# Optimization experiments

Measured on AMD Instinct MI355X. Metric: run time of the kernel, lower is better.

## Reference

```python
import jax, jax.numpy as jnp
import numpy as np

N_NODES = 50000
N_EDGES = 800000
NUM_HEADS = 4
HEAD_DIM = 32
IN_DIM = 128
NEG_SLOPE = 0.2


def setup_inputs() -> dict:
    key = jax.random.key(0)
    k1, k2, k3, k4, k5, k6 = jax.random.split(key, 6)
    x = jax.random.normal(k1, (N_NODES, IN_DIM), dtype=jnp.float32)
    W = jax.random.normal(k2, (NUM_HEADS * HEAD_DIM, IN_DIM), dtype=jnp.float32) * 0.05
    attn_l = jax.random.normal(k3, (NUM_HEADS, HEAD_DIM), dtype=jnp.float32) * 0.05
    attn_r = jax.random.normal(k4, (NUM_HEADS, HEAD_DIM), dtype=jnp.float32) * 0.05
    src = jax.random.randint(k5, (N_EDGES,), 0, N_NODES, dtype=jnp.int32)
    dst = jnp.sort(jax.random.randint(k6, (N_EDGES,), 0, N_NODES, dtype=jnp.int32))
    return {"x": x, "W": W, "attn_l": attn_l, "attn_r": attn_r, "src": src, "dst": dst}


def reference(x, W, attn_l, attn_r, src, dst):
    N = x.shape[0]
    H, D = attn_l.shape
    # linear projection: [N, H*D] -> [N, H, D]
    feat = (x @ W.T).reshape(N, H, D)
    # per-node attention terms  [N, H]
    el = jnp.einsum('nhd,hd->nh', feat, attn_l)
    er = jnp.einsum('nhd,hd->nh', feat, attn_r)
    # per-edge logits (u_add_v) + leaky relu  [E, H]
    e = el[src] + er[dst]
    e = jnp.where(e > 0, e, NEG_SLOPE * e)
    # edge softmax segmented by destination node
    e_max = jax.ops.segment_max(e, dst, num_segments=N)          # [N, H]
    e_exp = jnp.exp(e - e_max[dst])                              # [E, H]
    denom = jax.ops.segment_sum(e_exp, dst, num_segments=N)     # [N, H]
    alpha = e_exp / denom[dst]                                   # [E, H]
    # attention-weighted neighbor aggregation  [N, H, D]
    out = jax.ops.segment_sum(alpha[:, :, None] * feat[src], dst, num_segments=N)
    return out.reshape(N, H * D)
```

## Files before the change

kernel.cpp:

```cpp
#include <hip/hip_runtime.h>
#include <math.h>

#define NN 50000
#define NE 800000
#define NH 4
#define HD 32
#define FD 128
#define NTILE 3125
#define GEMM_BLOCKS 256
#define ROWS_BLOCKS ((NE + 511) / 512)
#define CAP 1024

typedef __attribute__((ext_vector_type(8))) short short8;
typedef __attribute__((ext_vector_type(4))) float floatx4;

__device__ __forceinline__ unsigned short f2bf(float f) {
    union { float f; unsigned u; } v; v.f = f;
    unsigned u = v.u;
    return (unsigned short)((u + 0x7FFFu + ((u >> 16) & 1u)) >> 16);
}
__device__ __forceinline__ float bf_lo(unsigned u) {
    union { unsigned u; float f; } v; v.u = u << 16; return v.f;
}
__device__ __forceinline__ float bf_hi(unsigned u) {
    union { unsigned u; float f; } v; v.u = u & 0xFFFF0000u; return v.f;
}

__global__ __launch_bounds__(512) void k_gemm_rows(const float* __restrict__ x,
                                                   const float* __restrict__ W,
                                                   const float* __restrict__ al,
                                                   const float* __restrict__ ar,
                                                   const int* __restrict__ dst,
                                                   unsigned short* __restrict__ feat_bf,
                                                   float* __restrict__ el,
                                                   float* __restrict__ er,
                                                   int* __restrict__ rows) {
    const int tid = threadIdx.x;

    if (blockIdx.x >= GEMM_BLOCKS) {
        int e = (blockIdx.x - GEMM_BLOCKS) * 512 + tid;
        if (e < NE) {
            int dj = dst[e];
            if (e == 0) {
                for (int n = 0; n <= dj; ++n) rows[n] = 0;
            } else {
                int prev = dst[e - 1];
                for (int n = prev + 1; n <= dj; ++n) rows[n] = e;
            }
            if (e == NE - 1) {
                for (int n = dj + 1; n <= NN; ++n) rows[n] = NE;
            }
        }
        return;
    }

    __shared__ unsigned short Wl[FD * 136];
    for (int p = tid; p < FD * 64; p += 512) {
        int c = p >> 6, k2 = (p & 63) * 2;
        float2 wv = *(const float2*)&W[c * FD + k2];
        *(unsigned*)&Wl[c * 136 + k2] =
            (unsigned)f2bf(wv.x) | ((unsigned)f2bf(wv.y) << 16);
    }
    __syncthreads();

    const int wv_id = tid >> 6, lane = tid & 63;
    const int col = lane & 15, quad = lane >> 4;

    float alr[8], arr[8];
    #pragma unroll
    for (int ct = 0; ct < 8; ++ct) {
        alr[ct] = al[col + 16 * ct];
        arr[ct] = ar[col + 16 * ct];
    }

    for (int tile = blockIdx.x * 8 + wv_id; tile < NTILE; tile += GEMM_BLOCKS * 8) {
        const int n0 = tile * 16;

        short8 afrag[4];
        const float* xrow = x + (size_t)(n0 + col) * FD;
        #pragma unroll
        for (int s = 0; s < 4; ++s) {
            float4 u0 = *(const float4*)&xrow[s * 32 + quad * 8];
            float4 u1 = *(const float4*)&xrow[s * 32 + quad * 8 + 4];
            short8 a;
            a[0] = (short)f2bf(u0.x); a[1] = (short)f2bf(u0.y);
            a[2] = (short)f2bf(u0.z); a[3] = (short)f2bf(u0.w);
            a[4] = (short)f2bf(u1.x); a[5] = (short)f2bf(u1.y);
            a[6] = (short)f2bf(u1.z); a[7] = (short)f2bf(u1.w);
            afrag[s] = a;
        }

        floatx4 acc[8];
        #pragma unroll
        for (int ct = 0; ct < 8; ++ct) acc[ct] = (floatx4){0.f, 0.f, 0.f, 0.f};

        #pragma unroll
        for (int ct = 0; ct < 8; ++ct) {
            #pragma unroll
            for (int s = 0; s < 4; ++s) {
                short8 b = *(const short8*)&Wl[(ct * 16 + col) * 136 + s * 32 + quad * 8];
                acc[ct] = __builtin_amdgcn_mfma_f32_16x16x32_bf16(afrag[s], b, acc[ct], 0, 0, 0);
            }
        }

        #pragma unroll
        for (int ct = 0; ct < 8; ++ct) {
            #pragma unroll
            for (int r = 0; r < 4; ++r) {
                feat_bf[(size_t)(n0 + quad * 4 + r) * FD + ct * 16 + col] = f2bf(acc[ct][r]);
            }
        }

        #pragma unroll
        for (int r = 0; r < 4; ++r) {
            float ev[8];
            #pragma unroll
            for (int hh = 0; hh < NH; ++hh) {
                ev[hh]     = acc[2 * hh][r] * alr[2 * hh] + acc[2 * hh + 1][r] * alr[2 * hh + 1];
                ev[4 + hh] = acc[2 * hh][r] * arr[2 * hh] + acc[2 * hh + 1][r] * arr[2 * hh + 1];
            }
            #pragma unroll
            for (int m = 1; m < 16; m <<= 1) {
                #pragma unroll
                for (int j = 0; j < 8; ++j) ev[j] += __shfl_xor(ev[j], m);
            }
            if (col == 0) {
                int n = n0 + quad * 4 + r;
                *(float4*)&el[n * NH] = make_float4(ev[0], ev[1], ev[2], ev[3]);
                *(float4*)&er[n * NH] = make_float4(ev[4], ev[5], ev[6], ev[7]);
            }
        }
    }
}

__global__ __launch_bounds__(256) void k_aggregate(const unsigned short* __restrict__ feat_bf,
                                                   const float* __restrict__ el,
                                                   const float* __restrict__ er,
                                                   const int* __restrict__ src,
                                                   const int* __restrict__ dst,
                                                   const int* __restrict__ rows,
                                                   float* __restrict__ out) {
    __shared__ float wS[CAP * NH];
    const int tid = threadIdx.x;
    const int wave = tid >> 6;
    const int lane = tid & 63;
    const int n0 = blockIdx.x * 4;
    const int n  = n0 + wave;

    const int s0 = __builtin_amdgcn_readfirstlane(rows[n0]);
    const int t3 = __builtin_amdgcn_readfirstlane(rows[n0 + 4]);
    const int s  = __builtin_amdgcn_readfirstlane(rows[n]);
    const int t  = __builtin_amdgcn_readfirstlane(rows[n + 1]);

    const int q  = lane >> 4;
    const int lp = lane & 15;
    const int h  = lp >> 2;
    const int dimoff = 8 * lp;

    float acc[8] = {0.f, 0.f, 0.f, 0.f, 0.f, 0.f, 0.f, 0.f};
    float den = 0.f;

    for (int c0 = s0; c0 < t3; c0 += CAP) {
        const int c1 = min(c0 + CAP, t3);

        for (int e = c0 + tid; e < c1; e += 256) {
            int sj = src[e], dj = dst[e];
            float4 l4 = *(const float4*)&el[sj * NH];
            float4 r4 = *(const float4*)&er[dj * NH];
            float4 w; float lg;
            lg = l4.x + r4.x; w.x = __expf(fmaxf(lg, 0.2f * lg));
            lg = l4.y + r4.y; w.y = __expf(fmaxf(lg, 0.2f * lg));
            lg = l4.z + r4.z; w.z = __expf(fmaxf(lg, 0.2f * lg));
            lg = l4.w + r4.w; w.w = __expf(fmaxf(lg, 0.2f * lg));
            *(float4*)&wS[(e - c0) * NH] = w;
        }
        __syncthreads();

        const int sb = max(s, c0), tb = min(t, c1);
        for (int e = (sb & ~3); e < tb; e += 16) {
            const int base = e + 4 * q;
            int sj4[4];
            const bool full4 = (base >= sb) && (base + 3 < tb);
            if (full4) {
                int4 sv = *(const int4*)&src[base];
                sj4[0] = sv.x; sj4[1] = sv.y; sj4[2] = sv.z; sj4[3] = sv.w;
            } else {
                #pragma unroll
                for (int u = 0; u < 4; ++u) {
                    int ei = base + u;
                    sj4[u] = (ei >= sb && ei < tb) ? src[ei] : 0;
                }
            }

            float wv4[4];
            uint4 uvv[4];
            #pragma unroll
            for (int u = 0; u < 4; ++u) {
                int ei = base + u;
                bool v = (ei >= sb) && (ei < tb);
                wv4[u] = v ? wS[(ei - c0) * NH + h] : 0.f;
                if (v) uvv[u] = *(const uint4*)&feat_bf[(size_t)sj4[u] * FD + dimoff];
            }

            #pragma unroll
            for (int u = 0; u < 4; ++u) {
                int ei = base + u;
                if (ei >= sb && ei < tb) {
                    float w = wv4[u];
                    uint4 uv = uvv[u];
                    acc[0] += w * bf_lo(uv.x); acc[1] += w * bf_hi(uv.x);
                    acc[2] += w * bf_lo(uv.y); acc[3] += w * bf_hi(uv.y);
                    acc[4] += w * bf_lo(uv.z); acc[5] += w * bf_hi(uv.z);
                    acc[6] += w * bf_lo(uv.w); acc[7] += w * bf_hi(uv.w);
                    den += w;
                }
            }
        }
        __syncthreads();
    }

    #pragma unroll
    for (int m = 16; m < 64; m <<= 1) {
        #pragma unroll
        for (int j = 0; j < 8; ++j) acc[j] += __shfl_xor(acc[j], m);
        den += __shfl_xor(den, m);
    }

    if (q == 0) {
        const float rden = (den > 0.f) ? 1.f / den : 0.f;
        float* op = out + (size_t)n * FD + dimoff;
        *(float4*)op       = make_float4(acc[0] * rden, acc[1] * rden, acc[2] * rden, acc[3] * rden);
        *(float4*)(op + 4) = make_float4(acc[4] * rden, acc[5] * rden, acc[6] * rden, acc[7] * rden);
    }
}

extern "C" void kernel_launch(void* const* d_in, const int* in_sizes, int n_in,
                              void* d_out, int out_size, void* d_ws, size_t ws_size,
                              hipStream_t stream) {
    const float* x  = (const float*)d_in[0];
    const float* W  = (const float*)d_in[1];
    const float* al = (const float*)d_in[2];
    const float* ar = (const float*)d_in[3];
    const int* src  = (const int*)d_in[4];
    const int* dst  = (const int*)d_in[5];
    float* out = (float*)d_out;

    unsigned short* feat_bf = (unsigned short*)d_ws;
    float* el = (float*)(feat_bf + (size_t)NN * FD);
    float* er = el + (size_t)NN * NH;
    int*   rows = (int*)(er + (size_t)NN * NH);

    k_gemm_rows<<<GEMM_BLOCKS + ROWS_BLOCKS, 512, 0, stream>>>(x, W, al, ar, dst,
                                                               feat_bf, el, er, rows);
    k_aggregate<<<NN / 4, 256, 0, stream>>>(feat_bf, el, er, src, dst, rows, out);
}
```

Baseline: 136.3 us.

## Fold attention vectors into projection MFMA, cache src indices in LDS

Precomputes W^T·attn_l and W^T·attn_r as an extra bf16 weight tile in shared memory, so el/er come from one extra MFMA per tile instead of a shuffle reduction. The GEMM block count is doubled to spread the tiles across more blocks. The aggregation kernel stores src indices in LDS during the weight pass, which removes the repeated global src reads and the alignment branches. The cost is an extra per-block precompute of the folded weights, more LDS, and slightly different rounding because the folded attention weights are held in bf16.

```diff
diff --git a/kernel.cpp b/kernel.cpp
--- a/kernel.cpp
+++ b/kernel.cpp
@@ -7,7 +7,7 @@
 #define HD 32
 #define FD 128
 #define NTILE 3125
-#define GEMM_BLOCKS 256
+#define GEMM_BLOCKS 512
 #define ROWS_BLOCKS ((NE + 511) / 512)
 #define CAP 1024
 
@@ -18,6 +18,9 @@
     union { float f; unsigned u; } v; v.f = f;
     unsigned u = v.u;
     return (unsigned short)((u + 0x7FFFu + ((u >> 16) & 1u)) >> 16);
+}
+__device__ __forceinline__ float bfu(unsigned short u) {
+    union { unsigned u; float f; } v; v.u = (unsigned)u << 16; return v.f;
 }
 __device__ __forceinline__ float bf_lo(unsigned u) {
     union { unsigned u; float f; } v; v.u = u << 16; return v.f;
@@ -55,23 +58,35 @@
     }
 
     __shared__ unsigned short Wl[FD * 136];
+    __shared__ unsigned short WaL[16 * 136];
+    __shared__ float aS[2 * FD];
+
     for (int p = tid; p < FD * 64; p += 512) {
         int c = p >> 6, k2 = (p & 63) * 2;
         float2 wv = *(const float2*)&W[c * FD + k2];
         *(unsigned*)&Wl[c * 136 + k2] =
             (unsigned)f2bf(wv.x) | ((unsigned)f2bf(wv.y) << 16);
     }
+    if (tid < FD) aS[tid] = al[tid];
+    else if (tid < 2 * FD) aS[tid] = ar[tid - FD];
+    __syncthreads();
+
+    for (int p = tid; p < 16 * FD; p += 512) {
+        int c = p >> 7, k = p & 127;
+        float v = 0.f;
+        if (c < 8) {
+            int h = c & 3;
+            const float* av = &aS[(c >> 2) * FD + h * HD];
+            const unsigned short* wl = &Wl[h * HD * 136 + k];
+            #pragma unroll 8
+            for (int d = 0; d < HD; ++d) v += bfu(wl[d * 136]) * av[d];
+        }
+        WaL[c * 136 + k] = f2bf(v);
+    }
     __syncthreads();
 
     const int wv_id = tid >> 6, lane = tid & 63;
     const int col = lane & 15, quad = lane >> 4;
-
-    float alr[8], arr[8];
-    #pragma unroll
-    for (int ct = 0; ct < 8; ++ct) {
-        alr[ct] = al[col + 16 * ct];
-        arr[ct] = ar[col + 16 * ct];
-    }
 
     for (int tile = blockIdx.x * 8 + wv_id; tile < NTILE; tile += GEMM_BLOCKS * 8) {
         const int n0 = tile * 16;
@@ -90,9 +105,10 @@
             afrag[s] = a;
         }
 
-        floatx4 acc[8];
+        floatx4 acc[8], acce;
         #pragma unroll
         for (int ct = 0; ct < 8; ++ct) acc[ct] = (floatx4){0.f, 0.f, 0.f, 0.f};
+        acce = (floatx4){0.f, 0.f, 0.f, 0.f};
 
         #pragma unroll
         for (int ct = 0; ct < 8; ++ct) {
@@ -102,6 +118,11 @@
                 acc[ct] = __builtin_amdgcn_mfma_f32_16x16x32_bf16(afrag[s], b, acc[ct], 0, 0, 0);
             }
         }
+        #pragma unroll
+        for (int s = 0; s < 4; ++s) {
+            short8 b = *(const short8*)&WaL[col * 136 + s * 32 + quad * 8];
+            acce = __builtin_amdgcn_mfma_f32_16x16x32_bf16(afrag[s], b, acce, 0, 0, 0);
+        }
 
         #pragma unroll
         for (int ct = 0; ct < 8; ++ct) {
@@ -110,25 +131,11 @@
                 feat_bf[(size_t)(n0 + quad * 4 + r) * FD + ct * 16 + col] = f2bf(acc[ct][r]);
             }
         }
-
         #pragma unroll
         for (int r = 0; r < 4; ++r) {
-            float ev[8];
-            #pragma unroll
-            for (int hh = 0; hh < NH; ++hh) {
-                ev[hh]     = acc[2 * hh][r] * alr[2 * hh] + acc[2 * hh + 1][r] * alr[2 * hh + 1];
-                ev[4 + hh] = acc[2 * hh][r] * arr[2 * hh] + acc[2 * hh + 1][r] * arr[2 * hh + 1];
-            }
-            #pragma unroll
-            for (int m = 1; m < 16; m <<= 1) {
-                #pragma unroll
-                for (int j = 0; j < 8; ++j) ev[j] += __shfl_xor(ev[j], m);
-            }
-            if (col == 0) {
-                int n = n0 + quad * 4 + r;
-                *(float4*)&el[n * NH] = make_float4(ev[0], ev[1], ev[2], ev[3]);
-                *(float4*)&er[n * NH] = make_float4(ev[4], ev[5], ev[6], ev[7]);
-            }
+            int n = n0 + quad * 4 + r;
+            if (col < 4)      el[n * NH + col]     = acce[r];
+            else if (col < 8) er[n * NH + col - 4] = acce[r];
         }
     }
 }
@@ -141,6 +148,7 @@
                                                    const int* __restrict__ rows,
                                                    float* __restrict__ out) {
     __shared__ float wS[CAP * NH];
+    __shared__ int   sS[CAP];
     const int tid = threadIdx.x;
     const int wave = tid >> 6;
     const int lane = tid & 63;
@@ -165,6 +173,7 @@
 
         for (int e = c0 + tid; e < c1; e += 256) {
             int sj = src[e], dj = dst[e];
+            sS[e - c0] = sj;
             float4 l4 = *(const float4*)&el[sj * NH];
             float4 r4 = *(const float4*)&er[dj * NH];
             float4 w; float lg;
@@ -177,35 +186,24 @@
         __syncthreads();
 
         const int sb = max(s, c0), tb = min(t, c1);
-        for (int e = (sb & ~3); e < tb; e += 16) {
+        for (int e = sb; e < tb; e += 16) {
             const int base = e + 4 * q;
-            int sj4[4];
-            const bool full4 = (base >= sb) && (base + 3 < tb);
-            if (full4) {
-                int4 sv = *(const int4*)&src[base];
-                sj4[0] = sv.x; sj4[1] = sv.y; sj4[2] = sv.z; sj4[3] = sv.w;
-            } else {
-                #pragma unroll
-                for (int u = 0; u < 4; ++u) {
-                    int ei = base + u;
-                    sj4[u] = (ei >= sb && ei < tb) ? src[ei] : 0;
-                }
-            }
-
             float wv4[4];
+            int   sj4[4];
             uint4 uvv[4];
             #pragma unroll
             for (int u = 0; u < 4; ++u) {
                 int ei = base + u;
-                bool v = (ei >= sb) && (ei < tb);
-                wv4[u] = v ? wS[(ei - c0) * NH + h] : 0.f;
+                bool v = ei < tb;
+                int ii = v ? (ei - c0) : 0;
+                sj4[u] = sS[ii];
+                wv4[u] = v ? wS[ii * NH + h] : 0.f;
                 if (v) uvv[u] = *(const uint4*)&feat_bf[(size_t)sj4[u] * FD + dimoff];
             }
-
             #pragma unroll
             for (int u = 0; u < 4; ++u) {
                 int ei = base + u;
-                if (ei >= sb && ei < tb) {
+                if (ei < tb) {
                     float w = wv4[u];
                     uint4 uv = uvv[u];
                     acc[0] += w * bf_lo(uv.x); acc[1] += w * bf_hi(uv.x);
```

After: 130.8 us. 4.0% less time.
